# Performance work log

Measured on AMD Instinct MI355X. Metric: run time of the kernel, lower is better.

The kernel has to match this reference:

```python
import jax, jax.numpy as jnp
import numpy as np

N_RAYS = 65536
N_SAMPLES = 2_097_152
HID = 64
L_PTS, L_DIR = 10, 4
STEP = 5e-3
WHITE_BKGD = True


def posenc(x, L):
    # x [..., 3] -> [..., 3 + 6L]
    freqs = (2.0 ** jnp.arange(L)).astype(x.dtype)            # [L]
    ang = x[..., None, :] * freqs[:, None]                     # [..., L, 3]
    enc = jnp.concatenate([jnp.sin(ang), jnp.cos(ang)], -1)   # [..., L, 6]
    return jnp.concatenate([x, enc.reshape(x.shape[:-1] + (6 * L,))], -1)


def setup_inputs() -> dict:
    key = jax.random.key(0)
    ks = jax.random.split(key, 12)
    rays_o = jax.random.normal(ks[0], (N_RAYS, 3), jnp.float32)
    viewdirs = jax.random.normal(ks[1], (N_RAYS, 3), jnp.float32)
    viewdirs = viewdirs / jnp.linalg.norm(viewdirs, axis=-1, keepdims=True)
    ray_indices = jnp.sort(jax.random.randint(ks[2], (N_SAMPLES,), 0, N_RAYS, jnp.int32))
    t_starts = jax.random.uniform(ks[3], (N_SAMPLES,), jnp.float32, 0.0, 4.0)
    t_ends = t_starts + STEP

    def w(k, shape):
        return jax.random.normal(k, shape, jnp.float32) / jnp.sqrt(shape[0])

    D_PTS = 3 + 6 * L_PTS   # 63
    D_DIR = 3 + 6 * L_DIR   # 27
    return dict(
        rays_o=rays_o, viewdirs=viewdirs, t_starts=t_starts, t_ends=t_ends,
        W1=w(ks[4], (D_PTS, HID)), b1=jnp.zeros((HID,), jnp.float32),
        W2=w(ks[5], (HID, HID)), b2=jnp.zeros((HID,), jnp.float32),
        Wd=w(ks[6], (HID, 1)), bd=jnp.zeros((1,), jnp.float32),
        Wf=w(ks[7], (HID, HID)), bf=jnp.zeros((HID,), jnp.float32),
        Wr1=w(ks[8], (HID + D_DIR, HID)), br1=jnp.zeros((HID,), jnp.float32),
        Wr2=w(ks[9], (HID, 3)), br2=jnp.zeros((3,), jnp.float32),
        ray_indices=ray_indices,
    )


def reference(rays_o, viewdirs, t_starts, t_ends,
              W1, b1, W2, b2, Wd, bd, Wf, bf, Wr1, br1, Wr2, br2,
              ray_indices):
    t_mid = 0.5 * (t_starts + t_ends)                     # [S]
    o = rays_o[ray_indices]                               # gather [S,3]
    d = viewdirs[ray_indices]                             # gather [S,3]
    pts = o + d * t_mid[:, None]                          # [S,3]

    # small NeRF MLP (self.net): sigma + view-dependent rgb
    h = jax.nn.relu(posenc(pts, L_PTS) @ W1 + b1)
    h = jax.nn.relu(h @ W2 + b2)
    sigma = jax.nn.relu((h @ Wd + bd)[:, 0])              # relu(density)
    feat = h @ Wf + bf
    hd = jax.nn.relu(jnp.concatenate([feat, posenc(d, L_DIR)], -1) @ Wr1 + br1)
    rgb = jax.nn.sigmoid(hd @ Wr2 + br2)                  # [S,3]

    alpha = 1.0 - jnp.exp(-sigma * (t_ends - t_starts))   # [S], in [0,1)

    # per-ray exclusive transmittance via segment exclusive cumsum in log space
    log1m = jnp.log1p(-jnp.clip(alpha, 0.0, 1.0 - 1e-7))  # <= 0
    excl = jnp.cumsum(log1m) - log1m                      # global exclusive cumsum
    counts = jax.ops.segment_sum(jnp.ones_like(ray_indices), ray_indices, N_RAYS)
    start_idx = jnp.cumsum(counts) - counts               # first sample of each ray
    offset = jnp.where(counts > 0, excl[jnp.clip(start_idx, 0, N_SAMPLES - 1)], 0.0)
    T = jnp.exp(excl - offset[ray_indices])               # transmittance [S]
    w = T * alpha                                         # render weights [S]

    colors = jax.ops.segment_sum(w[:, None] * rgb, ray_indices, N_RAYS)   # [R,3]
    opac = jax.ops.segment_sum(w, ray_indices, N_RAYS)                    # [R]
    depth = jax.ops.segment_sum(w * t_mid, ray_indices, N_RAYS)           # [R]

    bkgd = 1.0 if WHITE_BKGD else 0.0
    colors = colors + (1.0 - opac)[:, None] * bkgd
    return colors, opac[:, None], depth[:, None]
```

## Files before the change

### kernel.cpp

```cpp
#include <hip/hip_runtime.h>
#include <math.h>

#define NR 65536
#define NS 2097152

typedef __attribute__((ext_vector_type(4))) float f32x4;
typedef __attribute__((ext_vector_type(8))) short short8;

#define RSTRIDE 52
#define GSTRIDE (16 * 52 + 4)


__device__ __forceinline__ uint packbf(float a, float b) {
    __bf16 lo = (__bf16)a, hi = (__bf16)b;
    ushort ul = __builtin_bit_cast(ushort, lo);
    ushort uh = __builtin_bit_cast(ushort, hi);
    return (uint)ul | ((uint)uh << 16);
}
__device__ __forceinline__ float bflo(uint u) { return __builtin_bit_cast(float, u << 16); }

__global__ void init_bounds(int* __restrict__ start, int* __restrict__ end) {
    int r = blockIdx.x * blockDim.x + threadIdx.x;
    if (r < NR) { start[r] = 0; end[r] = 0; }
}

__global__ void find_bounds(const int* __restrict__ ridx,
                            int* __restrict__ start, int* __restrict__ end) {
    int i = blockIdx.x * blockDim.x + threadIdx.x;
    if (i >= NS) return;
    int r = ridx[i];
    if (i == 0 || ridx[i - 1] != r) start[r] = i;
    if (i == NS - 1 || ridx[i + 1] != r) end[r] = i + 1;
}

__global__ void build_frags(const float* __restrict__ W1, const float* __restrict__ W2,
                            const float* __restrict__ Wf, const float* __restrict__ Wr1,
                            const float* __restrict__ Wd, const float* __restrict__ Wr2,
                            uint4* __restrict__ wfrag) {
    int t = blockIdx.x * blockDim.x + threadIdx.x;
    if (t >= 40 * 64) return;
    int f = t >> 6, lane = t & 63;
    int c = lane & 15;
    uint q[4];
    if (f < 36) {
        const float* W; int kmax, fl;
        if (f < 8)       { W = W1;  kmax = 63; fl = f; }
        else if (f < 16) { W = W2;  kmax = 64; fl = f - 8; }
        else if (f < 24) { W = Wf;  kmax = 64; fl = f - 16; }
        else             { W = Wr1; kmax = 91; fl = f - 24; }
        int ks = fl >> 2, ft = fl & 3;
        int n = ft * 16 + c;
        int kb = ks * 32 + ((lane >> 4) * 8);
        #pragma unroll
        for (int j = 0; j < 4; ++j) {
            int k0 = kb + 2 * j, k1 = k0 + 1;
            float v0 = (k0 < kmax) ? W[k0 * 64 + n] : 0.0f;
            float v1 = (k1 < kmax) ? W[k1 * 64 + n] : 0.0f;
            q[j] = packbf(v0, v1);
        }
    } else if (f < 38) {
        int kb = (f - 36) * 32 + ((lane >> 4) * 8);
        #pragma unroll
        for (int j = 0; j < 4; ++j) {
            float v0 = (c == 0) ? Wd[kb + 2 * j] : 0.0f;
            float v1 = (c == 0) ? Wd[kb + 2 * j + 1] : 0.0f;
            q[j] = packbf(v0, v1);
        }
    } else {
        int kb = (f - 38) * 32 + ((lane >> 4) * 8);
        #pragma unroll
        for (int j = 0; j < 4; ++j) {
            float v0 = (c < 3) ? Wr2[(kb + 2 * j) * 3 + c] : 0.0f;
            float v1 = (c < 3) ? Wr2[(kb + 2 * j + 1) * 3 + c] : 0.0f;
            q[j] = packbf(v0, v1);
        }
    }
    wfrag[(size_t)f * 64 + lane] = make_uint4(q[0], q[1], q[2], q[3]);
}


template <int KS, bool RELU, bool SIGMA>
__device__ __forceinline__ void dense_layer(uint* S, const uint4* __restrict__ wfrag,
                                            int fb, const float* __restrict__ bias,
                                            float bd0, uint rbase, uint wbA, uint wbB,
                                            int lane, float* sigout) {
    const int g = lane >> 4;
    uint4 wf[KS * 4];
    #pragma unroll
    for (int i = 0; i < KS * 4; ++i) wf[i] = wfrag[(size_t)(fb + i) * 64 + lane];
    uint4 wsg[2];
    if constexpr (SIGMA) {
        wsg[0] = wfrag[36 * 64 + lane];
        wsg[1] = wfrag[37 * 64 + lane];
    }
    float4 bfr[4];
    #pragma unroll
    for (int ft = 0; ft < 4; ++ft)
        bfr[ft] = *(const float4*)(bias + 16 * ft + 4 * g);

    #pragma unroll
    for (int st = 0; st < 4; ++st) {
        const uint stoff = (uint)st * (uint)GSTRIDE;
        uint4 B[KS];
        #pragma unroll
        for (int ks = 0; ks < KS; ++ks)
            B[ks] = *(const uint4*)&S[rbase + stoff + 16u * (uint)ks];
        f32x4 acc[4];
        #pragma unroll
        for (int ft = 0; ft < 4; ++ft)
            acc[ft] = (f32x4){bfr[ft].x, bfr[ft].y, bfr[ft].z, bfr[ft].w};
        f32x4 sacc;
        if constexpr (SIGMA) sacc = (f32x4){(g == 0) ? bd0 : 0.0f, 0.0f, 0.0f, 0.0f};
        #pragma unroll
        for (int ks = 0; ks < KS; ++ks) {
            short8 bv = __builtin_bit_cast(short8, B[ks]);
            #pragma unroll
            for (int ft = 0; ft < 4; ++ft)
                acc[ft] = __builtin_amdgcn_mfma_f32_16x16x32_bf16(
                    __builtin_bit_cast(short8, wf[ks * 4 + ft]), bv, acc[ft], 0, 0, 0);
            if constexpr (SIGMA)
                sacc = __builtin_amdgcn_mfma_f32_16x16x32_bf16(
                    __builtin_bit_cast(short8, wsg[ks]), bv, sacc, 0, 0, 0);
        }
        #pragma unroll
        for (int ft = 0; ft < 4; ++ft) {
            float a0 = acc[ft][0], a1 = acc[ft][1], a2 = acc[ft][2], a3 = acc[ft][3];
            if constexpr (RELU) {
                a0 = fmaxf(a0, 0.0f); a1 = fmaxf(a1, 0.0f);
                a2 = fmaxf(a2, 0.0f); a3 = fmaxf(a3, 0.0f);
            }
            uint2 v = make_uint2(packbf(a0, a1), packbf(a2, a3));
            uint base = (ft & 1) ? wbB : wbA;
            *(uint2*)&S[base + stoff + 16u * (uint)(ft >> 1)] = v;
        }
        if constexpr (SIGMA) sigout[st] = sacc[0];
    }
}

__global__ __launch_bounds__(256, 3) void fused_mlp(
    const float* __restrict__ rays_o, const float* __restrict__ viewdirs,
    const float* __restrict__ t_starts, const float* __restrict__ t_ends,
    const float* __restrict__ b1, const float* __restrict__ b2,
    const float* __restrict__ bd, const float* __restrict__ bf_,
    const float* __restrict__ br1, const float* __restrict__ br2,
    const int* __restrict__ ridx, const uint4* __restrict__ wfrag,
    uint2* __restrict__ rgba)
{
    __shared__ uint S[16 * GSTRIDE];

    const int tid = threadIdx.x;
    const int w = tid >> 6, lane = tid & 63;
    const int g = lane >> 4, s = lane & 15;
    const uint wgb = (uint)(w * 4) * (uint)GSTRIDE;
    const uint rowcol = wgb + (uint)s * (uint)RSTRIDE;
    const int si = blockIdx.x * 256 + tid;

    int rr = ridx[si];
    float ts = t_starts[si], te = t_ends[si];
    float tm = 0.5f * (ts + te), dtv = te - ts;
    float dx = viewdirs[3 * rr + 0], dy = viewdirs[3 * rr + 1], dz = viewdirs[3 * rr + 2];
    float px = rays_o[3 * rr + 0] + dx * tm;
    float py = rays_o[3 * rr + 1] + dy * tm;
    float pz = rays_o[3 * rr + 2] + dz * tm;

    const uint ownrow = wgb + (uint)g * (uint)GSTRIDE + (uint)s * (uint)RSTRIDE;
    const uint rbase = rowcol + 4u * (uint)g;
    const uint wbA = rowcol + 2u * (uint)g;
    const uint wbB = wbA + 8u;

    {
        float enc[64];
        enc[0] = px; enc[1] = py; enc[2] = pz;
        float sx = __sinf(px), cx = __cosf(px);
        float sy = __sinf(py), cy = __cosf(py);
        float sz = __sinf(pz), cz = __cosf(pz);
        #pragma unroll
        for (int l = 0; l < 10; ++l) {
            enc[3 + 6 * l + 0] = sx; enc[3 + 6 * l + 1] = sy; enc[3 + 6 * l + 2] = sz;
            enc[3 + 6 * l + 3] = cx; enc[3 + 6 * l + 4] = cy; enc[3 + 6 * l + 5] = cz;
            float nsx = 2.0f * sx * cx, nsy = 2.0f * sy * cy, nsz = 2.0f * sz * cz;
            cx = fmaf(-2.0f * sx, sx, 1.0f);
            cy = fmaf(-2.0f * sy, sy, 1.0f);
            cz = fmaf(-2.0f * sz, sz, 1.0f);
            sx = nsx; sy = nsy; sz = nsz;
        }
        enc[63] = 0.0f;
        #pragma unroll
        for (int ch = 0; ch < 8; ++ch) {
            uint4 q = make_uint4(packbf(enc[8 * ch + 0], enc[8 * ch + 1]),
                                 packbf(enc[8 * ch + 2], enc[8 * ch + 3]),
                                 packbf(enc[8 * ch + 4], enc[8 * ch + 5]),
                                 packbf(enc[8 * ch + 6], enc[8 * ch + 7]));
            *(uint4*)&S[ownrow + 4u * (uint)ch] = q;
        }
    }
    {
        float de[32];
        de[0] = dx; de[1] = dy; de[2] = dz;
        float sx = __sinf(dx), cx = __cosf(dx);
        float sy = __sinf(dy), cy = __cosf(dy);
        float sz = __sinf(dz), cz = __cosf(dz);
        #pragma unroll
        for (int l = 0; l < 4; ++l) {
            de[3 + 6 * l + 0] = sx; de[3 + 6 * l + 1] = sy; de[3 + 6 * l + 2] = sz;
            de[3 + 6 * l + 3] = cx; de[3 + 6 * l + 4] = cy; de[3 + 6 * l + 5] = cz;
            float nsx = 2.0f * sx * cx, nsy = 2.0f * sy * cy, nsz = 2.0f * sz * cz;
            cx = fmaf(-2.0f * sx, sx, 1.0f);
            cy = fmaf(-2.0f * sy, sy, 1.0f);
            cz = fmaf(-2.0f * sz, sz, 1.0f);
            sx = nsx; sy = nsy; sz = nsz;
        }
        #pragma unroll
        for (int k = 27; k < 32; ++k) de[k] = 0.0f;
        #pragma unroll
        for (int c = 0; c < 4; ++c) {
            uint4 q = make_uint4(packbf(de[8 * c + 0], de[8 * c + 1]),
                                 packbf(de[8 * c + 2], de[8 * c + 3]),
                                 packbf(de[8 * c + 4], de[8 * c + 5]),
                                 packbf(de[8 * c + 6], de[8 * c + 7]));
            *(uint4*)&S[ownrow + 32u + 4u * (uint)c] = q;
        }
    }
    S[ownrow + 48] = __builtin_bit_cast(uint, dtv);

    float sig4[4];
    float bd0 = bd[0];

    dense_layer<2, true,  false>(S, wfrag,  0, b1,  0.0f, rbase, wbA, wbB, lane, sig4);
    dense_layer<2, true,  false>(S, wfrag,  8, b2,  0.0f, rbase, wbA, wbB, lane, sig4);
    dense_layer<2, false, true >(S, wfrag, 16, bf_, bd0,  rbase, wbA, wbB, lane, sig4);
    dense_layer<3, true,  false>(S, wfrag, 24, br1, 0.0f, rbase, wbA, wbB, lane, sig4);

    {
        uint4 wr0 = wfrag[38 * 64 + lane], wr1f = wfrag[39 * 64 + lane];
        float c0 = br2[0], c1 = br2[1], c2 = br2[2];
        #pragma unroll
        for (int st = 0; st < 4; ++st) {
            const uint stoff = (uint)st * (uint)GSTRIDE;
            uint4 B0 = *(const uint4*)&S[rbase + stoff];
            uint4 B1 = *(const uint4*)&S[rbase + stoff + 16u];
            f32x4 acc = (g == 0) ? (f32x4){c0, c1, c2, 0.0f}
                                 : (f32x4){0.0f, 0.0f, 0.0f, 0.0f};
            acc = __builtin_amdgcn_mfma_f32_16x16x32_bf16(
                __builtin_bit_cast(short8, wr0), __builtin_bit_cast(short8, B0), acc, 0, 0, 0);
            acc = __builtin_amdgcn_mfma_f32_16x16x32_bf16(
                __builtin_bit_cast(short8, wr1f), __builtin_bit_cast(short8, B1), acc, 0, 0, 0);
            if (lane < 16) {
                float sg = fmaxf(sig4[st], 0.0f);
                float dte = __builtin_bit_cast(float,
                    S[wgb + stoff + (uint)lane * (uint)RSTRIDE + 48u]);
                float alpha = 1.0f - __expf(-sg * dte);
                float r0 = 1.0f / (1.0f + __expf(-acc[0]));
                float r1 = 1.0f / (1.0f + __expf(-acc[1]));
                float r2 = 1.0f / (1.0f + __expf(-acc[2]));
                uint2 o;
                o.x = packbf(r0, r1);
                o.y = packbf(r2, alpha);
                rgba[blockIdx.x * 256 + w * 64 + st * 16 + lane] = o;
            }
        }
    }
}

__global__ void render_kernel(const uint2* __restrict__ rgba,
                              const float* __restrict__ t_starts,
                              const float* __restrict__ t_ends,
                              const int* __restrict__ start,
                              const int* __restrict__ end,
                              float* __restrict__ out)
{
    int r = blockIdx.x * blockDim.x + threadIdx.x;
    if (r >= NR) return;
    int sb = start[r], e = end[r];
    float T = 1.0f, c0 = 0.0f, c1 = 0.0f, c2 = 0.0f, op = 0.0f, dp = 0.0f;
    for (int i = sb; i < e; ++i) {
        uint2 q = rgba[i];
        float vr = bflo(q.x & 0xffffu), vg = bflo(q.x >> 16);
        float vb = bflo(q.y & 0xffffu), va = bflo(q.y >> 16);
        float wgt = T * va;
        float tmid = 0.5f * (t_starts[i] + t_ends[i]);
        c0 += wgt * vr; c1 += wgt * vg; c2 += wgt * vb;
        op += wgt; dp += wgt * tmid;
        T *= (1.0f - va);
    }
    float bg = 1.0f - op;
    c0 += bg; c1 += bg; c2 += bg;
    out[3 * r + 0] = c0;
    out[3 * r + 1] = c1;
    out[3 * r + 2] = c2;
    out[3 * NR + r] = op;
    out[4 * NR + r] = dp;
}

extern "C" void kernel_launch(void* const* d_in, const int* in_sizes, int n_in,
                              void* d_out, int out_size, void* d_ws, size_t ws_size,
                              hipStream_t stream) {
    const float* rays_o   = (const float*)d_in[0];
    const float* viewdirs = (const float*)d_in[1];
    const float* t_starts = (const float*)d_in[2];
    const float* t_ends   = (const float*)d_in[3];
    const float* W1  = (const float*)d_in[4];
    const float* b1  = (const float*)d_in[5];
    const float* W2  = (const float*)d_in[6];
    const float* b2  = (const float*)d_in[7];
    const float* Wd  = (const float*)d_in[8];
    const float* bd  = (const float*)d_in[9];
    const float* Wf  = (const float*)d_in[10];
    const float* bf_ = (const float*)d_in[11];
    const float* Wr1 = (const float*)d_in[12];
    const float* br1 = (const float*)d_in[13];
    const float* Wr2 = (const float*)d_in[14];
    const float* br2 = (const float*)d_in[15];
    const int* ridx  = (const int*)d_in[16];
    float* out = (float*)d_out;

    char* ws = (char*)d_ws;
    uint2* rgba = (uint2*)ws;
    int* start = (int*)(ws + (size_t)NS * 8);
    int* end   = start + NR;
    uint4* wfrag = (uint4*)(ws + (size_t)NS * 8 + (size_t)NR * 8);

    build_frags<<<10, 256, 0, stream>>>(W1, W2, Wf, Wr1, Wd, Wr2, wfrag);
    init_bounds<<<NR / 256, 256, 0, stream>>>(start, end);
    find_bounds<<<NS / 256, 256, 0, stream>>>(ridx, start, end);
    fused_mlp<<<NS / 256, 256, 0, stream>>>(
        rays_o, viewdirs, t_starts, t_ends,
        b1, b2, bd, bf_, br1, br2, ridx, wfrag, rgba);
    render_kernel<<<NR / 256, 256, 0, stream>>>(rgba, t_starts, t_ends, start, end, out);
}
```

Baseline: 167.0 us.

## Precompute per-ray direction encoding table and feed it directly as MFMA operand

Adds a per-ray kernel that computes the view-direction positional encoding once, packs it into bf16 and stores it in a workspace table. The fused MLP then gathers these packed fragments straight into registers as the last K-slice of the rgb layer, so the per-sample direction sin/cos work and its shared-memory staging go away. The shared-memory row stride shrinks accordingly, sigma is kept in LDS instead of registers, and launch bounds are raised to allow more resident blocks. In exchange it adds an extra kernel launch and a random gather of 64 bytes per sample from the direction table.

```diff
diff --git a/kernel.cpp b/kernel.cpp
--- a/kernel.cpp
+++ b/kernel.cpp
@@ -7,8 +7,8 @@
 typedef __attribute__((ext_vector_type(4))) float f32x4;
 typedef __attribute__((ext_vector_type(8))) short short8;
 
-#define RSTRIDE 52
-#define GSTRIDE (16 * 52 + 4)
+#define RSTRIDE 36
+#define GSTRIDE (16 * 36 + 4)
 
 
 __device__ __forceinline__ uint packbf(float a, float b) {
@@ -31,6 +31,38 @@
     int r = ridx[i];
     if (i == 0 || ridx[i - 1] != r) start[r] = i;
     if (i == NS - 1 || ridx[i + 1] != r) end[r] = i + 1;
+}
+
+__global__ void direnc_kernel(const float* __restrict__ viewdirs,
+                              uint4* __restrict__ dtab) {
+    int r = blockIdx.x * blockDim.x + threadIdx.x;
+    if (r >= NR) return;
+    float dx = viewdirs[3 * r + 0], dy = viewdirs[3 * r + 1], dz = viewdirs[3 * r + 2];
+    float de[32];
+    de[0] = dx; de[1] = dy; de[2] = dz;
+    float sx = __sinf(dx), cx = __cosf(dx);
+    float sy = __sinf(dy), cy = __cosf(dy);
+    float sz = __sinf(dz), cz = __cosf(dz);
+    #pragma unroll
+    for (int l = 0; l < 4; ++l) {
+        de[3 + 6 * l + 0] = sx; de[3 + 6 * l + 1] = sy; de[3 + 6 * l + 2] = sz;
+        de[3 + 6 * l + 3] = cx; de[3 + 6 * l + 4] = cy; de[3 + 6 * l + 5] = cz;
+        float nsx = 2.0f * sx * cx, nsy = 2.0f * sy * cy, nsz = 2.0f * sz * cz;
+        cx = fmaf(-2.0f * sx, sx, 1.0f);
+        cy = fmaf(-2.0f * sy, sy, 1.0f);
+        cz = fmaf(-2.0f * sz, sz, 1.0f);
+        sx = nsx; sy = nsy; sz = nsz;
+    }
+    #pragma unroll
+    for (int k = 27; k < 32; ++k) de[k] = 0.0f;
+    #pragma unroll
+    for (int c = 0; c < 4; ++c) {
+        uint4 q = make_uint4(packbf(de[8 * c + 0], de[8 * c + 1]),
+                             packbf(de[8 * c + 2], de[8 * c + 3]),
+                             packbf(de[8 * c + 4], de[8 * c + 5]),
+                             packbf(de[8 * c + 6], de[8 * c + 7]));
+        dtab[(size_t)r * 4 + c] = q;
+    }
 }
 
 __global__ void build_frags(const float* __restrict__ W1, const float* __restrict__ W2,
@@ -79,11 +111,11 @@
 }
 
 
-template <int KS, bool RELU, bool SIGMA>
+template <int KS, bool RELU, bool SIGMA, bool DIRB>
 __device__ __forceinline__ void dense_layer(uint* S, const uint4* __restrict__ wfrag,
                                             int fb, const float* __restrict__ bias,
                                             float bd0, uint rbase, uint wbA, uint wbB,
-                                            int lane, float* sigout) {
+                                            int lane, const uint4 (&dirB)[4]) {
     const int g = lane >> 4;
     uint4 wf[KS * 4];
     #pragma unroll
@@ -103,8 +135,10 @@
         const uint stoff = (uint)st * (uint)GSTRIDE;
         uint4 B[KS];
         #pragma unroll
-        for (int ks = 0; ks < KS; ++ks)
-            B[ks] = *(const uint4*)&S[rbase + stoff + 16u * (uint)ks];
+        for (int ks = 0; ks < KS; ++ks) {
+            if (DIRB && ks == KS - 1) B[ks] = dirB[st];
+            else B[ks] = *(const uint4*)&S[rbase + stoff + 16u * (uint)ks];
+        }
         f32x4 acc[4];
         #pragma unroll
         for (int ft = 0; ft < 4; ++ft)
@@ -133,18 +167,20 @@
             uint base = (ft & 1) ? wbB : wbA;
             *(uint2*)&S[base + stoff + 16u * (uint)(ft >> 1)] = v;
         }
-        if constexpr (SIGMA) sigout[st] = sacc[0];
-    }
-}
-
-__global__ __launch_bounds__(256, 3) void fused_mlp(
+        if constexpr (SIGMA) {
+            if (g == 0) S[rbase + stoff + 33u] = __builtin_bit_cast(uint, sacc[0]);
+        }
+    }
+}
+
+__global__ __launch_bounds__(256, 4) void fused_mlp(
     const float* __restrict__ rays_o, const float* __restrict__ viewdirs,
     const float* __restrict__ t_starts, const float* __restrict__ t_ends,
     const float* __restrict__ b1, const float* __restrict__ b2,
     const float* __restrict__ bd, const float* __restrict__ bf_,
     const float* __restrict__ br1, const float* __restrict__ br2,
     const int* __restrict__ ridx, const uint4* __restrict__ wfrag,
-    uint2* __restrict__ rgba)
+    const uint4* __restrict__ dtab, uint2* __restrict__ rgba)
 {
     __shared__ uint S[16 * GSTRIDE];
 
@@ -153,9 +189,17 @@
     const int g = lane >> 4, s = lane & 15;
     const uint wgb = (uint)(w * 4) * (uint)GSTRIDE;
     const uint rowcol = wgb + (uint)s * (uint)RSTRIDE;
-    const int si = blockIdx.x * 256 + tid;
-
-    int rr = ridx[si];
+    const int sb0 = blockIdx.x * 256 + w * 64;
+
+    int ridx4[4];
+    #pragma unroll
+    for (int st = 0; st < 4; ++st) ridx4[st] = ridx[sb0 + st * 16 + s];
+    uint4 dirB[4];
+    #pragma unroll
+    for (int st = 0; st < 4; ++st) dirB[st] = dtab[(size_t)ridx4[st] * 4 + g];
+
+    const int si = sb0 + g * 16 + s;
+    const int rr = ridx4[g];
     float ts = t_starts[si], te = t_ends[si];
     float tm = 0.5f * (ts + te), dtv = te - ts;
     float dx = viewdirs[3 * rr + 0], dy = viewdirs[3 * rr + 1], dz = viewdirs[3 * rr + 2];
@@ -194,42 +238,15 @@
             *(uint4*)&S[ownrow + 4u * (uint)ch] = q;
         }
     }
-    {
-        float de[32];
-        de[0] = dx; de[1] = dy; de[2] = dz;
-        float sx = __sinf(dx), cx = __cosf(dx);
-        float sy = __sinf(dy), cy = __cosf(dy);
-        float sz = __sinf(dz), cz = __cosf(dz);
-        #pragma unroll
-        for (int l = 0; l < 4; ++l) {
-            de[3 + 6 * l + 0] = sx; de[3 + 6 * l + 1] = sy; de[3 + 6 * l + 2] = sz;
-            de[3 + 6 * l + 3] = cx; de[3 + 6 * l + 4] = cy; de[3 + 6 * l + 5] = cz;
-            float nsx = 2.0f * sx * cx, nsy = 2.0f * sy * cy, nsz = 2.0f * sz * cz;
-            cx = fmaf(-2.0f * sx, sx, 1.0f);
-            cy = fmaf(-2.0f * sy, sy, 1.0f);
-            cz = fmaf(-2.0f * sz, sz, 1.0f);
-            sx = nsx; sy = nsy; sz = nsz;
-        }
-        #pragma unroll
-        for (int k = 27; k < 32; ++k) de[k] = 0.0f;
-        #pragma unroll
-        for (int c = 0; c < 4; ++c) {
-            uint4 q = make_uint4(packbf(de[8 * c + 0], de[8 * c + 1]),
-                                 packbf(de[8 * c + 2], de[8 * c + 3]),
-                                 packbf(de[8 * c + 4], de[8 * c + 5]),
-                                 packbf(de[8 * c + 6], de[8 * c + 7]));
-            *(uint4*)&S[ownrow + 32u + 4u * (uint)c] = q;
-        }
-    }
-    S[ownrow + 48] = __builtin_bit_cast(uint, dtv);
-
-    float sig4[4];
+    S[ownrow + 32] = __builtin_bit_cast(uint, dtv);
+
     float bd0 = bd[0];
-
-    dense_layer<2, true,  false>(S, wfrag,  0, b1,  0.0f, rbase, wbA, wbB, lane, sig4);
-    dense_layer<2, true,  false>(S, wfrag,  8, b2,  0.0f, rbase, wbA, wbB, lane, sig4);
-    dense_layer<2, false, true >(S, wfrag, 16, bf_, bd0,  rbase, wbA, wbB, lane, sig4);
-    dense_layer<3, true,  false>(S, wfrag, 24, br1, 0.0f, rbase, wbA, wbB, lane, sig4);
+    uint4 dummy[4];
+
+    dense_layer<2, true,  false, false>(S, wfrag,  0, b1,  0.0f, rbase, wbA, wbB, lane, dummy);
+    dense_layer<2, true,  false, false>(S, wfrag,  8, b2,  0.0f, rbase, wbA, wbB, lane, dummy);
+    dense_layer<2, false, true,  false>(S, wfrag, 16, bf_, bd0,  rbase, wbA, wbB, lane, dummy);
+    dense_layer<3, true,  false, true >(S, wfrag, 24, br1, 0.0f, rbase, wbA, wbB, lane, dirB);
 
     {
         uint4 wr0 = wfrag[38 * 64 + lane], wr1f = wfrag[39 * 64 + lane];
@@ -246,9 +263,8 @@
             acc = __builtin_amdgcn_mfma_f32_16x16x32_bf16(
                 __builtin_bit_cast(short8, wr1f), __builtin_bit_cast(short8, B1), acc, 0, 0, 0);
             if (lane < 16) {
-                float sg = fmaxf(sig4[st], 0.0f);
-                float dte = __builtin_bit_cast(float,
-                    S[wgb + stoff + (uint)lane * (uint)RSTRIDE + 48u]);
+                float sg = fmaxf(__builtin_bit_cast(float, S[rbase + stoff + 33u]), 0.0f);
+                float dte = __builtin_bit_cast(float, S[rbase + stoff + 32u]);
                 float alpha = 1.0f - __expf(-sg * dte);
                 float r0 = 1.0f / (1.0f + __expf(-acc[0]));
                 float r1 = 1.0f / (1.0f + __expf(-acc[1]));
@@ -256,7 +272,7 @@
                 uint2 o;
                 o.x = packbf(r0, r1);
                 o.y = packbf(r2, alpha);
-                rgba[blockIdx.x * 256 + w * 64 + st * 16 + lane] = o;
+                rgba[sb0 + st * 16 + lane] = o;
             }
         }
     }
@@ -319,12 +335,14 @@
     int* start = (int*)(ws + (size_t)NS * 8);
     int* end   = start + NR;
     uint4* wfrag = (uint4*)(ws + (size_t)NS * 8 + (size_t)NR * 8);
+    uint4* dtab  = (uint4*)(ws + (size_t)NS * 8 + (size_t)NR * 8 + 40 * 64 * 16);
 
     build_frags<<<10, 256, 0, stream>>>(W1, W2, Wf, Wr1, Wd, Wr2, wfrag);
+    direnc_kernel<<<NR / 256, 256, 0, stream>>>(viewdirs, dtab);
     init_bounds<<<NR / 256, 256, 0, stream>>>(start, end);
     find_bounds<<<NS / 256, 256, 0, stream>>>(ridx, start, end);
     fused_mlp<<<NS / 256, 256, 0, stream>>>(
         rays_o, viewdirs, t_starts, t_ends,
-        b1, b2, bd, bf_, br1, br2, ridx, wfrag, rgba);
+        b1, b2, bd, bf_, br1, br2, ridx, wfrag, dtab, rgba);
     render_kernel<<<NR / 256, 256, 0, stream>>>(rgba, t_starts, t_ends, start, end, out);
 }
```

Result: faster. 159.6 us (-4.4%).
